# Kernel optimization log

Measured on AMD Instinct MI355X. Metric: run time of the kernel, lower is better.

Reference implementation:

```python
import jax, jax.numpy as jnp
import numpy as np
import math

B, S, D, H = 2, 2048, 1024, 16
DK = D // H

def setup_inputs() -> dict:
    key = jax.random.key(0)
    ks = jax.random.split(key, 8)
    query = jax.random.normal(ks[0], (B, S, D), dtype=jnp.float32)
    k_in = jax.random.normal(ks[1], (B, S, D), dtype=jnp.float32)
    value = jax.random.normal(ks[2], (B, S, D), dtype=jnp.float32)
    mask = jax.random.randint(ks[3], (B, S, S), 0, 2, dtype=jnp.int32)
    scale = 1.0 / math.sqrt(D)
    Wq = jax.random.normal(ks[4], (D, D), dtype=jnp.float32) * scale
    Wk = jax.random.normal(ks[5], (D, D), dtype=jnp.float32) * scale
    Wv = jax.random.normal(ks[6], (D, D), dtype=jnp.float32) * scale
    Wo = jax.random.normal(ks[7], (D, D), dtype=jnp.float32) * scale
    return {"query": query, "key": k_in, "value": value, "mask": mask,
            "Wq": Wq, "Wk": Wk, "Wv": Wv, "Wo": Wo}

def reference(query, key, value, mask, Wq, Wk, Wv, Wo):
    # torch Linear(no bias): y = x @ W.T ; weights are [out, in]
    def split_heads(x):  # [B,S,D] -> [B,H,S,DK]
        return x.reshape(B, S, H, DK).transpose(0, 2, 1, 3)
    q = split_heads(query @ Wq.T)
    k = split_heads(key @ Wk.T)
    v = split_heads(value @ Wv.T)
    scores = jnp.einsum('bhqd,bhkd->bhqk', q, k) / jnp.sqrt(jnp.float32(DK))
    scores = jnp.where(mask[:, None, :, :] == 0, jnp.float32(-1e9), scores)
    p_attn = jax.nn.softmax(scores, axis=-1)  # dropout is identity in eval mode
    attn = jnp.einsum('bhqk,bhkd->bhqd', p_attn, v)
    out = attn.transpose(0, 2, 1, 3).reshape(B, S, D)
    return out @ Wo.T
```

## Files before the change

kernel.cpp:

```cpp
#include <hip/hip_runtime.h>
#include <hip/hip_bf16.h>
#include <cstdint>
#include <cstddef>

constexpr int BATCH = 2;
constexpr int SEQ   = 2048;
constexpr int DIM   = 1024;
constexpr int NH    = 16;
constexpr int DK    = 64;

typedef unsigned short u16;
typedef unsigned int   u32;
typedef unsigned long long u64;

typedef __attribute__((ext_vector_type(8))) short bf16x8;
typedef __attribute__((ext_vector_type(8))) unsigned short u16x8;
typedef __attribute__((ext_vector_type(4))) float f32x4;
typedef __attribute__((ext_vector_type(16))) float f32x16;
typedef __attribute__((ext_vector_type(4))) unsigned int u32x4;

__device__ __forceinline__ u16 f2bf(float f) {
  u32 u = __builtin_bit_cast(u32, f);
  u32 r = (u + 0x7FFFu + ((u >> 16) & 1u)) >> 16;
  return (u16)r;
}

__device__ __forceinline__ u32 pack_bf2(float a, float b) {
  __hip_bfloat162 h2 = __float22bfloat162_rn(make_float2(a, b));
  u32 r;
  __builtin_memcpy(&r, &h2, 4);
  return r;
}

__device__ __forceinline__ float fexp2(float x) {
#if __has_builtin(__builtin_amdgcn_exp2f)
  return __builtin_amdgcn_exp2f(x);
#else
  return exp2f(x);
#endif
}

__device__ __forceinline__ void gload16(const u16* g, u16* l) {
  __builtin_amdgcn_global_load_lds(
      (const __attribute__((address_space(1))) void*)g,
      (__attribute__((address_space(3))) void*)l, 16, 0, 0);
}

__global__ __launch_bounds__(256) void cvt_bf16(const float* __restrict__ q,
                                                const float* __restrict__ k,
                                                const float* __restrict__ v,
                                                const float* __restrict__ wq,
                                                const float* __restrict__ wk,
                                                const float* __restrict__ wv,
                                                const float* __restrict__ wo,
                                                u16* __restrict__ dst) {
  constexpr size_t QS = (size_t)BATCH * SEQ * DIM;
  constexpr size_t WS = (size_t)DIM * DIM;
  const size_t i = ((size_t)blockIdx.x * 256 + threadIdx.x) * 8;
  const float* s;
  if      (i < QS)          s = q  + i;
  else if (i < 2 * QS)      s = k  + (i - QS);
  else if (i < 3 * QS)      s = v  + (i - 2 * QS);
  else if (i < 3 * QS + WS)     s = wq + (i - 3 * QS);
  else if (i < 3 * QS + 2 * WS) s = wk + (i - 3 * QS - WS);
  else if (i < 3 * QS + 3 * WS) s = wv + (i - 3 * QS - 2 * WS);
  else                          s = wo + (i - 3 * QS - 3 * WS);
  f32x4 a = *(const f32x4*)s, b2 = *(const f32x4*)(s + 4);
  u32x4 t;
  t[0] = pack_bf2(a[0], a[1]);  t[1] = pack_bf2(a[2], a[3]);
  t[2] = pack_bf2(b2[0], b2[1]); t[3] = pack_bf2(b2[2], b2[3]);
  *(u16x8*)(dst + i) = __builtin_bit_cast(u16x8, t);
}

__global__ __launch_bounds__(256) void pack_mask(const int* __restrict__ mask,
                                                 u64* __restrict__ bits) {
  int gt = blockIdx.x * 256 + threadIdx.x;
  u64 m = __ballot(mask[gt] != 0);
  if ((threadIdx.x & 63) == 0) bits[gt >> 6] = m;
}

__global__ __launch_bounds__(256) void transpose_v(const u16* __restrict__ V,
                                                   u16* __restrict__ Vt) {
  __shared__ u16 t[64][68];
  const int st = blockIdx.x * 64;
  const int bh = blockIdx.y;
  const int b = bh >> 4, h = bh & 15;
  const int tid = threadIdx.x;
#pragma unroll
  for (int s = 0; s < 2; ++s) {
    int c = tid + s * 256;
    int row = c >> 3, c8 = c & 7;
    u16x8 vv = *(const u16x8*)(V + ((size_t)(b * SEQ + st + row)) * DIM + h * DK + c8 * 8);
#pragma unroll
    for (int j = 0; j < 8; ++j) t[row][c8 * 8 + j] = vv[j];
  }
  __syncthreads();
#pragma unroll
  for (int s = 0; s < 2; ++s) {
    int c = tid + s * 256;
    int dk = c >> 3, sc = c & 7;
    u16x8 ov;
#pragma unroll
    for (int j = 0; j < 8; ++j) ov[j] = t[sc * 8 + j][dk];
    *(u16x8*)(Vt + ((size_t)bh * DK + dk) * SEQ + st + sc * 8) = ov;
  }
}

struct GemmParams {
  const void* A[3];
  const void* B[3];
  void*       C[3];
  float       alpha[3];
};

template <bool OUTF32>
__global__ __launch_bounds__(256) void gemm_nt(GemmParams p, int M, int N, int K) {
  const int z = blockIdx.z;
  __shared__ __align__(16) u16 As[128 * 32];
  __shared__ __align__(16) u16 Bs[128 * 32];

  const int tid = threadIdx.x;
  const int lane = tid & 63, w = tid >> 6;
  const int bm = blockIdx.y * 128, bn = blockIdx.x * 128;
  const int wm = (w >> 1) * 64, wn = (w & 1) * 64;
  const int ar = lane & 15, g = lane >> 4;

  const u16* A = (const u16*)p.A[z];
  const u16* B = (const u16*)p.B[z];

  const int sr0 = w * 32 + (lane >> 2);
  const int scol = (lane & 3) * 8;
  u16* const lA0 = &As[(w * 32) * 32];
  u16* const lA1 = &As[(w * 32 + 16) * 32];
  u16* const lB0 = &Bs[(w * 32) * 32];
  u16* const lB1 = &Bs[(w * 32 + 16) * 32];

  f32x4 acc[4][4] = {};

  for (int k0 = 0; k0 < K; k0 += 32) {
    gload16(&A[(size_t)(bm + sr0) * K + k0 + scol],      lA0);
    gload16(&A[(size_t)(bm + sr0 + 16) * K + k0 + scol], lA1);
    gload16(&B[(size_t)(bn + sr0) * K + k0 + scol],      lB0);
    gload16(&B[(size_t)(bn + sr0 + 16) * K + k0 + scol], lB1);
    __syncthreads();

    bf16x8 af[4], bfr[4];
#pragma unroll
    for (int m = 0; m < 4; ++m)
      af[m] = *(const bf16x8*)&As[(wm + m * 16 + ar) * 32 + g * 8];
#pragma unroll
    for (int n = 0; n < 4; ++n)
      bfr[n] = *(const bf16x8*)&Bs[(wn + n * 16 + ar) * 32 + g * 8];
#pragma unroll
    for (int m = 0; m < 4; ++m)
#pragma unroll
      for (int n = 0; n < 4; ++n)
        acc[m][n] = __builtin_amdgcn_mfma_f32_16x16x32_bf16(af[m], bfr[n], acc[m][n], 0, 0, 0);
    __syncthreads();
  }

  const float alpha = p.alpha[z];
#pragma unroll
  for (int m = 0; m < 4; ++m)
#pragma unroll
    for (int n = 0; n < 4; ++n)
#pragma unroll
      for (int r = 0; r < 4; ++r) {
        int row = bm + wm + m * 16 + g * 4 + r;
        int col = bn + wn + n * 16 + ar;
        float val = acc[m][n][r] * alpha;
        if (OUTF32) ((float*)p.C[z])[(size_t)row * N + col] = val;
        else        ((u16*)p.C[z])[(size_t)row * N + col]  = f2bf(val);
      }
}

__global__ __launch_bounds__(512, 2) void attn_fwd(const u16* __restrict__ Qb,
                                                   const u16* __restrict__ Kb,
                                                   const u16* __restrict__ Vtb,
                                                   const u64* __restrict__ mbits,
                                                   u16* __restrict__ Ob) {
  const int h = blockIdx.y, b = blockIdx.z;
  const int tid = threadIdx.x;
  const int lane = tid & 63, w = tid >> 6;
  const int l31 = lane & 31, hi = lane >> 5;
  const int half = w >> 2, wq = w & 3;

  __shared__ __align__(16) u16 SB[2 * 16384];
  __shared__ float Lsh[4][64];

  const int q0 = blockIdx.x * 128 + wq * 32;
  const int rsw = l31 & 7;

  bf16x8 qreg[4];
  {
    const u16* qp = Qb + ((size_t)(b * SEQ + q0 + l31)) * DIM + h * DK + 8 * hi;
#pragma unroll
    for (int s = 0; s < 4; ++s) qreg[s] = *(const bf16x8*)(qp + 16 * s);
  }

  const int grow = (w << 3) + (lane >> 3);
  const int gchk = (lane & 7) ^ (grow & 7);
  const u16* kbase  = Kb + ((size_t)b * SEQ + grow) * DIM + h * DK + gchk * 8;
  const u16* vtbase = Vtb + ((size_t)(b * NH + h) * DK + grow) * SEQ + gchk * 8;
  const u64* mrow   = mbits + (size_t)(b * SEQ + q0 + l31) * (SEQ / 64) + half * 16;

  f32x16 o[2] = {};
  float lsum = 0.f;

  {
    u16* const nb = SB;
    gload16(kbase,                          nb + 0     + w * 512);
    gload16(kbase + (size_t)1024 * DIM,     nb + 4096  + w * 512);
    gload16(vtbase,                         nb + 8192  + w * 512);
    gload16(vtbase + 1024,                  nb + 12288 + w * 512);
  }
  u64 mbc = mrow[0];
  __syncthreads();

  for (int kt = 0; kt < 16; ++kt) {
    const int cur = kt & 1;
    u64 mbn = mbc;
    if (kt < 15) {
      u16* const nb = SB + (cur ^ 1) * 16384;
      const u16* ks = kbase + (size_t)(kt + 1) * 64 * DIM;
      const u16* vs = vtbase + (kt + 1) * 64;
      gload16(ks,                       nb + 0     + w * 512);
      gload16(ks + (size_t)1024 * DIM,  nb + 4096  + w * 512);
      gload16(vs,                       nb + 8192  + w * 512);
      gload16(vs + 1024,                nb + 12288 + w * 512);
      mbn = mrow[kt + 1];
    }
    const u16* const Kc = SB + cur * 16384 + half * 4096;
    const u16* const Vc = SB + cur * 16384 + 8192 + half * 4096;

    const u64 nmb = ~mbc;
    const u64 mbh = nmb >> (hi * 4);
    const u32 nm[2] = {(u32)mbh, (u32)(mbh >> 32)};
    f32x16 sc[2];
#pragma unroll
    for (int kb = 0; kb < 2; ++kb)
#pragma unroll
      for (int r = 0; r < 16; ++r) {
        const int key = (r & 3) + 8 * (r >> 2);
        u32 t = (u32)(((int)(nm[kb] << (31 - key))) >> 31) & 0xC6EA6000u;
        sc[kb][r] = __builtin_bit_cast(float, t);
      }

#pragma unroll
    for (int kb = 0; kb < 2; ++kb) {
      const int row = kb * 32 + l31;
#pragma unroll
      for (int s = 0; s < 4; ++s) {
        bf16x8 kf = *(const bf16x8*)&Kc[row * 64 + ((2 * s + hi) ^ rsw) * 8];
        sc[kb] = __builtin_amdgcn_mfma_f32_32x32x16_bf16(kf, qreg[s], sc[kb], 0, 0, 0);
      }
    }

#pragma unroll
    for (int kb = 0; kb < 2; ++kb)
#pragma unroll
      for (int r = 0; r < 16; ++r)
        sc[kb][r] = fexp2(sc[kb][r]);
    float s8[8];
#pragma unroll
    for (int i = 0; i < 8; ++i)
      s8[i] = (sc[0][i] + sc[0][i + 8]) + (sc[1][i] + sc[1][i + 8]);
    lsum += ((s8[0] + s8[1]) + (s8[2] + s8[3])) + ((s8[4] + s8[5]) + (s8[6] + s8[7]));

#pragma unroll
    for (int kb = 0; kb < 2; ++kb) {
      u32 wv[8];
#pragma unroll
      for (int t = 0; t < 8; ++t)
        wv[t] = pack_bf2(sc[kb][2 * t], sc[kb][2 * t + 1]);
      u32 xa = (u32)__shfl_xor((int)(hi ? wv[0] : wv[2]), 32, 64);
      u32 xb = (u32)__shfl_xor((int)(hi ? wv[1] : wv[3]), 32, 64);
      u32 xc = (u32)__shfl_xor((int)(hi ? wv[4] : wv[6]), 32, 64);
      u32 xd = (u32)__shfl_xor((int)(hi ? wv[5] : wv[7]), 32, 64);
      u32x4 f0, f1;
      f0[0] = hi ? xa : wv[0];  f0[1] = hi ? xb : wv[1];
      f0[2] = hi ? wv[2] : xa;  f0[3] = hi ? wv[3] : xb;
      f1[0] = hi ? xc : wv[4];  f1[1] = hi ? xd : wv[5];
      f1[2] = hi ? wv[6] : xc;  f1[3] = hi ? wv[7] : xd;
      bf16x8 pa0 = __builtin_bit_cast(bf16x8, f0);
      bf16x8 pa1 = __builtin_bit_cast(bf16x8, f1);
#pragma unroll
      for (int ks = 0; ks < 2; ++ks) {
        bf16x8 pf = ks ? pa1 : pa0;
#pragma unroll
        for (int d = 0; d < 2; ++d) {
          const int row = l31 + 32 * d;
          bf16x8 vf = *(const bf16x8*)&Vc[row * 64 + ((4 * kb + 2 * ks + hi) ^ rsw) * 8];
          o[d] = __builtin_amdgcn_mfma_f32_32x32x16_bf16(pf, vf, o[d], 0, 0, 0);
        }
      }
    }
    mbc = mbn;
    __syncthreads();
  }

  lsum += __shfl_xor(lsum, 32, 64);
  f32x4* const oa4 = (f32x4*)SB;
  if (half == 1) {
    f32x4* dst = oa4 + (size_t)(wq * 64 + lane) * 8;
#pragma unroll
    for (int d = 0; d < 2; ++d)
#pragma unroll
      for (int cc = 0; cc < 4; ++cc) {
        f32x4 t = {o[d][cc * 4 + 0], o[d][cc * 4 + 1], o[d][cc * 4 + 2], o[d][cc * 4 + 3]};
        dst[(d * 4 + cc) ^ (lane & 7)] = t;
      }
    Lsh[wq][lane] = lsum;
  }
  __syncthreads();
  if (half == 0) {
    const float ltot = lsum + Lsh[wq][lane];
    const float linv = 1.0f / ltot;
    const f32x4* src = oa4 + (size_t)(wq * 64 + lane) * 8;
    f32x4 ov[8];
#pragma unroll
    for (int c = 0; c < 8; ++c) ov[c] = src[c ^ (lane & 7)];
    float lr[16];
#pragma unroll
    for (int r = 0; r < 16; ++r)
      lr[r] = __shfl(linv, (r & 3) + 8 * (r >> 2) + 4 * hi, 64);
#pragma unroll
    for (int d = 0; d < 2; ++d)
#pragma unroll
      for (int r = 0; r < 16; ++r) {
        const float om = o[d][r] + ov[d * 4 + (r >> 2)][r & 3];
        const int qloc = (r & 3) + 8 * (r >> 2) + 4 * hi;
        Ob[(size_t)(b * SEQ + q0 + qloc) * DIM + h * DK + l31 + 32 * d] = f2bf(om * lr[r]);
      }
  }
}

extern "C" void kernel_launch(void* const* d_in, const int* in_sizes, int n_in,
                              void* d_out, int out_size, void* d_ws, size_t ws_size,
                              hipStream_t stream) {
  const float* q    = (const float*)d_in[0];
  const float* k    = (const float*)d_in[1];
  const float* v    = (const float*)d_in[2];
  const int*   mask = (const int*)d_in[3];
  const float* Wq   = (const float*)d_in[4];
  const float* Wk   = (const float*)d_in[5];
  const float* Wv   = (const float*)d_in[6];
  const float* Wo   = (const float*)d_in[7];
  float* out = (float*)d_out;

  constexpr size_t QS = (size_t)BATCH * SEQ * DIM;
  constexpr size_t WSZ = (size_t)DIM * DIM;

  char* ws = (char*)d_ws;
  u64* mbits = (u64*)ws;
  u16* XB  = (u16*)(ws + 0x0100000);
  u16* xq = XB, *xk = XB + QS, *xv = XB + 2 * QS;
  u16* wqb = XB + 3 * QS, *wkb = wqb + WSZ, *wvb = wkb + WSZ, *wob = wvb + WSZ;
  u16* Qb  = (u16*)(ws + 0x2100000);
  u16* Kb  = (u16*)(ws + 0x2900000);
  u16* Vb  = (u16*)(ws + 0x3100000);
  u16* Vtb = (u16*)(ws + 0x3900000);
  u16* Ab  = (u16*)(ws + 0x4100000);

  cvt_bf16<<<(3 * QS + 4 * WSZ) / (256 * 8), 256, 0, stream>>>(q, k, v, Wq, Wk, Wv, Wo, XB);

  pack_mask<<<(BATCH * SEQ * SEQ) / 256, 256, 0, stream>>>(mask, mbits);

  GemmParams gp;
  gp.A[0] = xq;  gp.A[1] = xk;  gp.A[2] = xv;
  gp.B[0] = wqb; gp.B[1] = wkb; gp.B[2] = wvb;
  gp.C[0] = Qb;  gp.C[1] = Kb;  gp.C[2] = Vb;
  gp.alpha[0] = 0.125f * 1.44269504088896f; gp.alpha[1] = 1.0f; gp.alpha[2] = 1.0f;
  gemm_nt<false><<<dim3(DIM / 128, (BATCH * SEQ) / 128, 3), 256, 0, stream>>>(
      gp, BATCH * SEQ, DIM, DIM);

  transpose_v<<<dim3(SEQ / 64, BATCH * NH), 256, 0, stream>>>(Vb, Vtb);

  attn_fwd<<<dim3(SEQ / 128, NH, BATCH), 512, 0, stream>>>(Qb, Kb, Vtb, mbits, Ab);

  GemmParams go;
  go.A[0] = Ab; go.B[0] = wob; go.C[0] = out; go.alpha[0] = 1.0f;
  go.A[1] = go.A[2] = nullptr; go.B[1] = go.B[2] = nullptr; go.C[1] = go.C[2] = nullptr;
  go.alpha[1] = go.alpha[2] = 1.0f;
  gemm_nt<true><<<dim3(DIM / 128, (BATCH * SEQ) / 128, 1), 256, 0, stream>>>(
      go, BATCH * SEQ, DIM, DIM);
}
```

Before: 158.5 us.

## Merge prep kernels, use 32x32 MFMA in GEMM, permlane swap in attention

Combines the bf16 conversion and mask bit-packing into one launch to cut a kernel launch and allow the two to overlap. Switches the projection GEMM from 16x16x32 to 32x32x16 MFMA tiles, which needs fewer LDS fragment loads per MFMA. Replaces the shuffle-and-select exchange in the attention P-fragment build with v_permlane32_swap. Each is a separate local optimisation, and the inline asm relies on an instruction available on this architecture.

```diff
diff --git a/kernel.cpp b/kernel.cpp
--- a/kernel.cpp
+++ b/kernel.cpp
@@ -40,43 +40,52 @@
 #endif
 }
 
+__device__ __forceinline__ void plswap32(u32& a, u32& b) {
+  asm volatile("v_permlane32_swap_b32 %0, %1" : "+v"(a), "+v"(b));
+}
+
 __device__ __forceinline__ void gload16(const u16* g, u16* l) {
   __builtin_amdgcn_global_load_lds(
       (const __attribute__((address_space(1))) void*)g,
       (__attribute__((address_space(3))) void*)l, 16, 0, 0);
 }
 
-__global__ __launch_bounds__(256) void cvt_bf16(const float* __restrict__ q,
-                                                const float* __restrict__ k,
-                                                const float* __restrict__ v,
-                                                const float* __restrict__ wq,
-                                                const float* __restrict__ wk,
-                                                const float* __restrict__ wv,
-                                                const float* __restrict__ wo,
-                                                u16* __restrict__ dst) {
-  constexpr size_t QS = (size_t)BATCH * SEQ * DIM;
-  constexpr size_t WS = (size_t)DIM * DIM;
-  const size_t i = ((size_t)blockIdx.x * 256 + threadIdx.x) * 8;
-  const float* s;
-  if      (i < QS)          s = q  + i;
-  else if (i < 2 * QS)      s = k  + (i - QS);
-  else if (i < 3 * QS)      s = v  + (i - 2 * QS);
-  else if (i < 3 * QS + WS)     s = wq + (i - 3 * QS);
-  else if (i < 3 * QS + 2 * WS) s = wk + (i - 3 * QS - WS);
-  else if (i < 3 * QS + 3 * WS) s = wv + (i - 3 * QS - 2 * WS);
-  else                          s = wo + (i - 3 * QS - 3 * WS);
-  f32x4 a = *(const f32x4*)s, b2 = *(const f32x4*)(s + 4);
-  u32x4 t;
-  t[0] = pack_bf2(a[0], a[1]);  t[1] = pack_bf2(a[2], a[3]);
-  t[2] = pack_bf2(b2[0], b2[1]); t[3] = pack_bf2(b2[2], b2[3]);
-  *(u16x8*)(dst + i) = __builtin_bit_cast(u16x8, t);
-}
-
-__global__ __launch_bounds__(256) void pack_mask(const int* __restrict__ mask,
-                                                 u64* __restrict__ bits) {
-  int gt = blockIdx.x * 256 + threadIdx.x;
-  u64 m = __ballot(mask[gt] != 0);
-  if ((threadIdx.x & 63) == 0) bits[gt >> 6] = m;
+constexpr size_t QS  = (size_t)BATCH * SEQ * DIM;
+constexpr size_t WSZ = (size_t)DIM * DIM;
+constexpr int CVT_BLOCKS  = (int)((3 * QS + 4 * WSZ) / (256 * 8));
+constexpr int MASK_BLOCKS = (BATCH * SEQ * SEQ) / 256;
+
+__global__ __launch_bounds__(256) void prep(const float* __restrict__ q,
+                                            const float* __restrict__ k,
+                                            const float* __restrict__ v,
+                                            const float* __restrict__ wq,
+                                            const float* __restrict__ wk,
+                                            const float* __restrict__ wv,
+                                            const float* __restrict__ wo,
+                                            u16* __restrict__ dst,
+                                            const int* __restrict__ mask,
+                                            u64* __restrict__ bits) {
+  const int bid = blockIdx.x;
+  if (bid < CVT_BLOCKS) {
+    const size_t i = ((size_t)bid * 256 + threadIdx.x) * 8;
+    const float* s;
+    if      (i < QS)              s = q  + i;
+    else if (i < 2 * QS)          s = k  + (i - QS);
+    else if (i < 3 * QS)          s = v  + (i - 2 * QS);
+    else if (i < 3 * QS + WSZ)     s = wq + (i - 3 * QS);
+    else if (i < 3 * QS + 2 * WSZ) s = wk + (i - 3 * QS - WSZ);
+    else if (i < 3 * QS + 3 * WSZ) s = wv + (i - 3 * QS - 2 * WSZ);
+    else                           s = wo + (i - 3 * QS - 3 * WSZ);
+    f32x4 a = *(const f32x4*)s, b2 = *(const f32x4*)(s + 4);
+    u32x4 t;
+    t[0] = pack_bf2(a[0], a[1]);  t[1] = pack_bf2(a[2], a[3]);
+    t[2] = pack_bf2(b2[0], b2[1]); t[3] = pack_bf2(b2[2], b2[3]);
+    *(u16x8*)(dst + i) = __builtin_bit_cast(u16x8, t);
+  } else {
+    const int gt = (bid - CVT_BLOCKS) * 256 + threadIdx.x;
+    u64 m = __ballot(mask[gt] != 0);
+    if ((threadIdx.x & 63) == 0) bits[gt >> 6] = m;
+  }
 }
 
 __global__ __launch_bounds__(256) void transpose_v(const u16* __restrict__ V,
@@ -121,9 +130,9 @@
 
   const int tid = threadIdx.x;
   const int lane = tid & 63, w = tid >> 6;
+  const int l31 = lane & 31, hi = lane >> 5;
   const int bm = blockIdx.y * 128, bn = blockIdx.x * 128;
   const int wm = (w >> 1) * 64, wn = (w & 1) * 64;
-  const int ar = lane & 15, g = lane >> 4;
 
   const u16* A = (const u16*)p.A[z];
   const u16* B = (const u16*)p.B[z];
@@ -135,7 +144,7 @@
   u16* const lB0 = &Bs[(w * 32) * 32];
   u16* const lB1 = &Bs[(w * 32 + 16) * 32];
 
-  f32x4 acc[4][4] = {};
+  f32x16 acc[2][2] = {};
 
   for (int k0 = 0; k0 < K; k0 += 32) {
     gload16(&A[(size_t)(bm + sr0) * K + k0 + scol],      lA0);
@@ -144,31 +153,34 @@
     gload16(&B[(size_t)(bn + sr0 + 16) * K + k0 + scol], lB1);
     __syncthreads();
 
-    bf16x8 af[4], bfr[4];
-#pragma unroll
-    for (int m = 0; m < 4; ++m)
-      af[m] = *(const bf16x8*)&As[(wm + m * 16 + ar) * 32 + g * 8];
-#pragma unroll
-    for (int n = 0; n < 4; ++n)
-      bfr[n] = *(const bf16x8*)&Bs[(wn + n * 16 + ar) * 32 + g * 8];
-#pragma unroll
-    for (int m = 0; m < 4; ++m)
-#pragma unroll
-      for (int n = 0; n < 4; ++n)
-        acc[m][n] = __builtin_amdgcn_mfma_f32_16x16x32_bf16(af[m], bfr[n], acc[m][n], 0, 0, 0);
+#pragma unroll
+    for (int ks = 0; ks < 2; ++ks) {
+      bf16x8 af[2], bf[2];
+#pragma unroll
+      for (int mb = 0; mb < 2; ++mb)
+        af[mb] = *(const bf16x8*)&As[(wm + mb * 32 + l31) * 32 + ks * 16 + hi * 8];
+#pragma unroll
+      for (int nb = 0; nb < 2; ++nb)
+        bf[nb] = *(const bf16x8*)&Bs[(wn + nb * 32 + l31) * 32 + ks * 16 + hi * 8];
+#pragma unroll
+      for (int mb = 0; mb < 2; ++mb)
+#pragma unroll
+        for (int nb = 0; nb < 2; ++nb)
+          acc[mb][nb] = __builtin_amdgcn_mfma_f32_32x32x16_bf16(af[mb], bf[nb], acc[mb][nb], 0, 0, 0);
+    }
     __syncthreads();
   }
 
   const float alpha = p.alpha[z];
 #pragma unroll
-  for (int m = 0; m < 4; ++m)
-#pragma unroll
-    for (int n = 0; n < 4; ++n)
-#pragma unroll
-      for (int r = 0; r < 4; ++r) {
-        int row = bm + wm + m * 16 + g * 4 + r;
-        int col = bn + wn + n * 16 + ar;
-        float val = acc[m][n][r] * alpha;
+  for (int mb = 0; mb < 2; ++mb)
+#pragma unroll
+    for (int nb = 0; nb < 2; ++nb)
+#pragma unroll
+      for (int r = 0; r < 16; ++r) {
+        const int row = bm + wm + mb * 32 + (r & 3) + 8 * (r >> 2) + 4 * hi;
+        const int col = bn + wn + nb * 32 + l31;
+        float val = acc[mb][nb][r] * alpha;
         if (OUTF32) ((float*)p.C[z])[(size_t)row * N + col] = val;
         else        ((u16*)p.C[z])[(size_t)row * N + col]  = f2bf(val);
       }
@@ -273,15 +285,12 @@
 #pragma unroll
       for (int t = 0; t < 8; ++t)
         wv[t] = pack_bf2(sc[kb][2 * t], sc[kb][2 * t + 1]);
-      u32 xa = (u32)__shfl_xor((int)(hi ? wv[0] : wv[2]), 32, 64);
-      u32 xb = (u32)__shfl_xor((int)(hi ? wv[1] : wv[3]), 32, 64);
-      u32 xc = (u32)__shfl_xor((int)(hi ? wv[4] : wv[6]), 32, 64);
-      u32 xd = (u32)__shfl_xor((int)(hi ? wv[5] : wv[7]), 32, 64);
-      u32x4 f0, f1;
-      f0[0] = hi ? xa : wv[0];  f0[1] = hi ? xb : wv[1];
-      f0[2] = hi ? wv[2] : xa;  f0[3] = hi ? wv[3] : xb;
-      f1[0] = hi ? xc : wv[4];  f1[1] = hi ? xd : wv[5];
-      f1[2] = hi ? wv[6] : xc;  f1[3] = hi ? wv[7] : xd;
+      plswap32(wv[0], wv[2]);
+      plswap32(wv[1], wv[3]);
+      plswap32(wv[4], wv[6]);
+      plswap32(wv[5], wv[7]);
+      u32x4 f0 = {wv[0], wv[1], wv[2], wv[3]};
+      u32x4 f1 = {wv[4], wv[5], wv[6], wv[7]};
       bf16x8 pa0 = __builtin_bit_cast(bf16x8, f0);
       bf16x8 pa1 = __builtin_bit_cast(bf16x8, f1);
 #pragma unroll
@@ -348,9 +357,6 @@
   const float* Wo   = (const float*)d_in[7];
   float* out = (float*)d_out;
 
-  constexpr size_t QS = (size_t)BATCH * SEQ * DIM;
-  constexpr size_t WSZ = (size_t)DIM * DIM;
-
   char* ws = (char*)d_ws;
   u64* mbits = (u64*)ws;
   u16* XB  = (u16*)(ws + 0x0100000);
@@ -362,9 +368,8 @@
   u16* Vtb = (u16*)(ws + 0x3900000);
   u16* Ab  = (u16*)(ws + 0x4100000);
 
-  cvt_bf16<<<(3 * QS + 4 * WSZ) / (256 * 8), 256, 0, stream>>>(q, k, v, Wq, Wk, Wv, Wo, XB);
-
-  pack_mask<<<(BATCH * SEQ * SEQ) / 256, 256, 0, stream>>>(mask, mbits);
+  prep<<<CVT_BLOCKS + MASK_BLOCKS, 256, 0, stream>>>(q, k, v, Wq, Wk, Wv, Wo, XB,
+                                                     mask, mbits);
 
   GemmParams gp;
   gp.A[0] = xq;  gp.A[1] = xk;  gp.A[2] = xv;
```

After: 155.1 us. 2.2% less time.
